# Performance work log

Measured on AMD Instinct MI355X. Metric: run time of the kernel, lower is better.

Reference implementation:

```python
import jax, jax.numpy as jnp
import numpy as np

TEMP = 0.07
WEIGHT = 0.5
EPS = 1e-8  # matches torch F.cosine_similarity norm clamp


def setup_inputs() -> dict:
    key = jax.random.key(0)
    k1, k2, k3 = jax.random.split(key, 3)
    B, T, D = 64, 512, 512
    video = jax.random.normal(k1, (B, T, D), dtype=jnp.float32)
    audio = jax.random.normal(k2, (B, T, D), dtype=jnp.float32)
    mask = jax.random.randint(k3, (B, T), 0, 2, dtype=jnp.int32)
    return {"video": video, "audio": audio, "mask": mask}


def reference(video, audio, mask):
    B, T, D = video.shape
    # L2-normalize features (cosine similarity = dot of normalized vectors)
    vn = video / jnp.clip(jnp.linalg.norm(video, axis=-1, keepdims=True), EPS)
    an = audio / jnp.clip(jnp.linalg.norm(audio, axis=-1, keepdims=True), EPS)
    idx = jnp.argmax(mask, axis=1)                                   # [B]
    a_anchor = jnp.take_along_axis(an, idx[:, None, None], axis=1)[:, 0]  # [B,D]
    v_anchor = jnp.take_along_axis(vn, idx[:, None, None], axis=1)[:, 0]  # [B,D]
    # scaled cosine sims of all timesteps vs the anchor of the other modality
    sims_a2v = jnp.einsum('btd,bd->bt', vn, a_anchor) / TEMP         # cos(v_j, a_idx)/T
    sims_v2a = jnp.einsum('btd,bd->bt', an, v_anchor) / TEMP         # cos(a_j, v_idx)/T
    # positive: cos(v_idx, a_idx)/T (same for both directions)
    pos = jnp.take_along_axis(sims_a2v, idx[:, None], axis=1)[:, 0]  # [B]
    not_pos = jnp.arange(T)[None, :] != idx[:, None]                 # [B,T]
    neg_a = jnp.sum(jnp.where(not_pos, jnp.exp(sims_a2v), 0.0), axis=1)  # a2v negatives
    neg_v = jnp.sum(jnp.where(not_pos, jnp.exp(sims_v2a), 0.0), axis=1)  # v2a negatives
    pos_exp = jnp.exp(pos)
    batch_loss_a = jnp.sum(-jnp.log(pos_exp / neg_a))
    batch_loss_v = jnp.sum(-jnp.log(pos_exp / neg_v))
    return ((batch_loss_a * WEIGHT + batch_loss_v * WEIGHT) / B).reshape(1)
```

## Files before the change

### kernel.cpp

```cpp
#include <hip/hip_runtime.h>
#include <math.h>

#define TEMP_INV (1.0f / 0.07f)
#define WEIGHT 0.5f
#define EPS 1e-8f
#define BB 64
#define TT 512
#define DD 512
#define RR 4
#define NC 4
#define ROWS_PER_WAVE (RR * NC)
#define XBLK (TT / (4 * ROWS_PER_WAVE))
#define NBLK (XBLK * BB * 2)
#define IDX_INF 0x7fffffff

typedef float f32x4 __attribute__((ext_vector_type(4)));

__device__ inline float wave_sum(float v) {
    for (int o = 32; o >= 1; o >>= 1) v += __shfl_xor(v, o, 64);
    return v;
}
__device__ inline int wave_min_i(int v) {
    for (int o = 32; o >= 1; o >>= 1) v = min(v, __shfl_xor(v, o, 64));
    return v;
}

#define LOADC(B0, B1, CH)                                                   \
    _Pragma("unroll")                                                       \
    for (int r = 0; r < RR; r++) {                                          \
        const float* row_ = base + (size_t)(t0 + (CH) * RR + r) * DD;       \
        B0[r] = *(const f32x4*)(row_ + lane * 4);                           \
        B1[r] = *(const f32x4*)(row_ + 256 + lane * 4);                     \
    }

#define COMPC(B0, B1, CH)                                                   \
    _Pragma("unroll")                                                       \
    for (int r = 0; r < RR; r++) {                                          \
        const int k_ = (CH) * RR + r;                                       \
        dot[k_] = B0[r].x * c0.x + B0[r].y * c0.y + B0[r].z * c0.z          \
                + B0[r].w * c0.w + B1[r].x * c1.x + B1[r].y * c1.y          \
                + B1[r].z * c1.z + B1[r].w * c1.w;                          \
        nrm[k_] = B0[r].x * B0[r].x + B0[r].y * B0[r].y + B0[r].z * B0[r].z \
                + B0[r].w * B0[r].w + B1[r].x * B1[r].x + B1[r].y * B1[r].y \
                + B1[r].z * B1[r].z + B1[r].w * B1[r].w;                    \
    }

__global__ __launch_bounds__(256) void fused_kernel(
    const float* __restrict__ video, const float* __restrict__ audio,
    const int* __restrict__ mask,
    float* __restrict__ pos, float* __restrict__ part,
    unsigned int* __restrict__ counter, float* __restrict__ out)
{
    const int b = blockIdx.y;
    const int dir = blockIdx.z;
    const int tid = threadIdx.x;
    const int wid = tid >> 6, lane = tid & 63;
    const int t0 = blockIdx.x * (4 * ROWS_PER_WAVE) + wid * ROWS_PER_WAVE;

    __shared__ int sh_i[4];
    __shared__ float sh_f[4][3];
    __shared__ int s_idx;
    __shared__ float s_anc[DD];
    __shared__ float s_inv;
    __shared__ int s_last;

    const float* base = (dir == 0 ? video : audio) + (size_t)b * TT * DD;

    int m0 = mask[b * TT + tid];
    int m1 = mask[b * TT + tid + 256];

    f32x4 pa0[RR], pa1[RR], pb0[RR], pb1[RR];
    LOADC(pa0, pa1, 0)
    LOADC(pb0, pb1, 1)
    asm volatile("" ::: "memory");

    int cand = min(m0 ? tid : IDX_INF, m1 ? (tid + 256) : IDX_INF);
    cand = wave_min_i(cand);
    if (lane == 0) sh_i[wid] = cand;
    __syncthreads();
    if (tid == 0) {
        int r = sh_i[0];
        for (int i = 1; i < 4; i++) r = min(r, sh_i[i]);
        s_idx = (r == IDX_INF) ? 0 : r;
    }
    __syncthreads();
    const int idx = s_idx;

    const float* ancrow = (dir == 0 ? audio : video) + (size_t)(b * TT + idx) * DD;

    float a0 = ancrow[tid], a1 = ancrow[tid + 256];
    s_anc[tid] = a0;
    s_anc[tid + 256] = a1;
    float ss = a0 * a0 + a1 * a1;
    float sso = 0.0f, dav = 0.0f;
    const bool posduty = (blockIdx.x == 0) && (dir == 0);
    ss = wave_sum(ss);
    if (posduty) {
        const float* vrow = video + (size_t)(b * TT + idx) * DD;
        float o0 = vrow[tid], o1 = vrow[tid + 256];
        sso = wave_sum(o0 * o0 + o1 * o1);
        dav = wave_sum(a0 * o0 + a1 * o1);
    }
    if (lane == 0) { sh_f[wid][0] = ss; sh_f[wid][1] = sso; sh_f[wid][2] = dav; }
    __syncthreads();
    if (tid == 0) {
        float ra = 0.f, ro = 0.f, rd = 0.f;
        for (int i = 0; i < 4; i++) { ra += sh_f[i][0]; ro += sh_f[i][1]; rd += sh_f[i][2]; }
        float inva = 1.0f / fmaxf(sqrtf(ra), EPS);
        s_inv = inva;
        if (posduty) {
            float invo = 1.0f / fmaxf(sqrtf(ro), EPS);
            __hip_atomic_store(&pos[b], rd * inva * invo * TEMP_INV,
                               __ATOMIC_RELAXED, __HIP_MEMORY_SCOPE_AGENT);
        }
    }
    __syncthreads();
    const float inv = s_inv;
    f32x4 c0 = ((const f32x4*)s_anc)[lane] * inv;
    f32x4 c1 = ((const f32x4*)(s_anc + 256))[lane] * inv;

    float dot[ROWS_PER_WAVE], nrm[ROWS_PER_WAVE];

    COMPC(pa0, pa1, 0)
    LOADC(pa0, pa1, 2)
    COMPC(pb0, pb1, 1)
    LOADC(pb0, pb1, 3)
    COMPC(pa0, pa1, 2)
    COMPC(pb0, pb1, 3)

#pragma unroll
    for (int o = 32; o >= 1; o >>= 1) {
#pragma unroll
        for (int k = 0; k < ROWS_PER_WAVE; k++) {
            dot[k] += __shfl_xor(dot[k], o, 64);
            nrm[k] += __shfl_xor(nrm[k], o, 64);
        }
    }

    if (lane == 0) {
        float local = 0.0f;
#pragma unroll
        for (int k = 0; k < ROWS_PER_WAVE; k++) {
            const int t = t0 + k;
            float sim = dot[k] / fmaxf(sqrtf(nrm[k]), EPS) * TEMP_INV;
            local += (t == idx) ? 0.0f : expf(sim);
        }
        sh_f[wid][0] = local;
    }
    __syncthreads();
    if (tid == 0) {
        float p = sh_f[0][0] + sh_f[1][0] + sh_f[2][0] + sh_f[3][0];
        const int bid_flat = (dir * BB + b) * XBLK + blockIdx.x;
        __hip_atomic_store(&part[bid_flat], p,
                           __ATOMIC_RELAXED, __HIP_MEMORY_SCOPE_AGENT);
        asm volatile("s_waitcnt vmcnt(0)" ::: "memory");
        unsigned old = __hip_atomic_fetch_add(counter, 1u,
                                              __ATOMIC_RELAXED, __HIP_MEMORY_SCOPE_AGENT);
        s_last = (old == (unsigned)(NBLK - 1)) ? 1 : 0;
    }
    __syncthreads();
    if (s_last && wid == 0) {
        float na = 0.f, nv = 0.f;
#pragma unroll
        for (int x = 0; x < XBLK; x++)
            na += __hip_atomic_load(&part[(0 * BB + lane) * XBLK + x],
                                    __ATOMIC_RELAXED, __HIP_MEMORY_SCOPE_AGENT);
#pragma unroll
        for (int x = 0; x < XBLK; x++)
            nv += __hip_atomic_load(&part[(1 * BB + lane) * XBLK + x],
                                    __ATOMIC_RELAXED, __HIP_MEMORY_SCOPE_AGENT);
        float p = __hip_atomic_load(&pos[lane],
                                    __ATOMIC_RELAXED, __HIP_MEMORY_SCOPE_AGENT);
        float term = WEIGHT * (logf(na) + logf(nv)) - p;
        term = wave_sum(term);
        if (lane == 0) out[0] = term * (1.0f / (float)BB);
    }
}

extern "C" void kernel_launch(void* const* d_in, const int* in_sizes, int n_in,
                              void* d_out, int out_size, void* d_ws, size_t ws_size,
                              hipStream_t stream)
{
    const float* video = (const float*)d_in[0];
    const float* audio = (const float*)d_in[1];
    const int* mask = (const int*)d_in[2];

    float* ws = (float*)d_ws;
    float* pos = ws;
    float* part = ws + BB;
    unsigned int* counter = (unsigned int*)(part + NBLK);

    hipMemsetAsync(counter, 0, sizeof(unsigned int), stream);

    dim3 grid(XBLK, BB, 2);
    fused_kernel<<<grid, 256, 0, stream>>>(video, audio, mask, pos, part, counter, (float*)d_out);
}
```

Baseline: 158.2 us.

## Split feature dimension across wave pairs and halve rows per block

Each block now covers 32 timesteps instead of 64, which doubles the grid. Wave pairs split the 512-wide feature dimension in half, and their partial dot products and norms are combined through shared memory before the exp. The aim is more resident waves and fewer registers per wave, so more memory parallelism can hide load latency. The row prefetch that used to be issued before the mask argmin and anchor normalisation now starts only after them, so that overlap is lost. Mask and anchor reads repeat in twice as many blocks.

```diff
diff --git a/kernel.cpp b/kernel.cpp
--- a/kernel.cpp
+++ b/kernel.cpp
@@ -8,9 +8,9 @@
 #define TT 512
 #define DD 512
 #define RR 4
-#define NC 4
-#define ROWS_PER_WAVE (RR * NC)
-#define XBLK (TT / (4 * ROWS_PER_WAVE))
+#define KROWS 16
+#define TROWS 32
+#define XBLK (TT / TROWS)
 #define NBLK (XBLK * BB * 2)
 #define IDX_INF 0x7fffffff
 
@@ -25,24 +25,20 @@
     return v;
 }
 
-#define LOADC(B0, B1, CH)                                                   \
+#define LOADC(BUF, CH)                                                      \
     _Pragma("unroll")                                                       \
     for (int r = 0; r < RR; r++) {                                          \
-        const float* row_ = base + (size_t)(t0 + (CH) * RR + r) * DD;       \
-        B0[r] = *(const f32x4*)(row_ + lane * 4);                           \
-        B1[r] = *(const f32x4*)(row_ + 256 + lane * 4);                     \
+        BUF[r] = *(const f32x4*)(base + (size_t)(rbase + (CH) * RR + r) * DD + coff); \
     }
 
-#define COMPC(B0, B1, CH)                                                   \
+#define COMPC(BUF, CH)                                                      \
     _Pragma("unroll")                                                       \
     for (int r = 0; r < RR; r++) {                                          \
         const int k_ = (CH) * RR + r;                                       \
-        dot[k_] = B0[r].x * c0.x + B0[r].y * c0.y + B0[r].z * c0.z          \
-                + B0[r].w * c0.w + B1[r].x * c1.x + B1[r].y * c1.y          \
-                + B1[r].z * c1.z + B1[r].w * c1.w;                          \
-        nrm[k_] = B0[r].x * B0[r].x + B0[r].y * B0[r].y + B0[r].z * B0[r].z \
-                + B0[r].w * B0[r].w + B1[r].x * B1[r].x + B1[r].y * B1[r].y \
-                + B1[r].z * B1[r].z + B1[r].w * B1[r].w;                    \
+        dot[k_] = BUF[r].x * c.x + BUF[r].y * c.y                           \
+                + BUF[r].z * c.z + BUF[r].w * c.w;                          \
+        nrm[k_] = BUF[r].x * BUF[r].x + BUF[r].y * BUF[r].y                 \
+                + BUF[r].z * BUF[r].z + BUF[r].w * BUF[r].w;                \
     }
 
 __global__ __launch_bounds__(256) void fused_kernel(
@@ -55,10 +51,13 @@
     const int dir = blockIdx.z;
     const int tid = threadIdx.x;
     const int wid = tid >> 6, lane = tid & 63;
-    const int t0 = blockIdx.x * (4 * ROWS_PER_WAVE) + wid * ROWS_PER_WAVE;
+    const int half = wid & 1;
+    const int rbase = blockIdx.x * TROWS + (wid >> 1) * KROWS;
+    const int coff = half * 256 + lane * 4;
 
     __shared__ int sh_i[4];
     __shared__ float sh_f[4][3];
+    __shared__ float s_red[4][KROWS][2];
     __shared__ int s_idx;
     __shared__ float s_anc[DD];
     __shared__ float s_inv;
@@ -68,33 +67,24 @@
 
     int m0 = mask[b * TT + tid];
     int m1 = mask[b * TT + tid + 256];
-
-    f32x4 pa0[RR], pa1[RR], pb0[RR], pb1[RR];
-    LOADC(pa0, pa1, 0)
-    LOADC(pb0, pb1, 1)
-    asm volatile("" ::: "memory");
-
     int cand = min(m0 ? tid : IDX_INF, m1 ? (tid + 256) : IDX_INF);
     cand = wave_min_i(cand);
     if (lane == 0) sh_i[wid] = cand;
     __syncthreads();
     if (tid == 0) {
-        int r = sh_i[0];
-        for (int i = 1; i < 4; i++) r = min(r, sh_i[i]);
+        int r = min(min(sh_i[0], sh_i[1]), min(sh_i[2], sh_i[3]));
         s_idx = (r == IDX_INF) ? 0 : r;
     }
     __syncthreads();
     const int idx = s_idx;
 
     const float* ancrow = (dir == 0 ? audio : video) + (size_t)(b * TT + idx) * DD;
-
     float a0 = ancrow[tid], a1 = ancrow[tid + 256];
     s_anc[tid] = a0;
     s_anc[tid + 256] = a1;
-    float ss = a0 * a0 + a1 * a1;
+    float ss = wave_sum(a0 * a0 + a1 * a1);
     float sso = 0.0f, dav = 0.0f;
     const bool posduty = (blockIdx.x == 0) && (dir == 0);
-    ss = wave_sum(ss);
     if (posduty) {
         const float* vrow = video + (size_t)(b * TT + idx) * DD;
         float o0 = vrow[tid], o1 = vrow[tid + 256];
@@ -116,40 +106,52 @@
     }
     __syncthreads();
     const float inv = s_inv;
-    f32x4 c0 = ((const f32x4*)s_anc)[lane] * inv;
-    f32x4 c1 = ((const f32x4*)(s_anc + 256))[lane] * inv;
+    f32x4 c = ((const f32x4*)s_anc)[half * 64 + lane] * inv;
 
-    float dot[ROWS_PER_WAVE], nrm[ROWS_PER_WAVE];
+    f32x4 pa[RR], pb[RR];
+    float dot[KROWS], nrm[KROWS];
 
-    COMPC(pa0, pa1, 0)
-    LOADC(pa0, pa1, 2)
-    COMPC(pb0, pb1, 1)
-    LOADC(pb0, pb1, 3)
-    COMPC(pa0, pa1, 2)
-    COMPC(pb0, pb1, 3)
+    LOADC(pa, 0)
+    LOADC(pb, 1)
+    COMPC(pa, 0)
+    LOADC(pa, 2)
+    COMPC(pb, 1)
+    LOADC(pb, 3)
+    COMPC(pa, 2)
+    COMPC(pb, 3)
 
 #pragma unroll
     for (int o = 32; o >= 1; o >>= 1) {
 #pragma unroll
-        for (int k = 0; k < ROWS_PER_WAVE; k++) {
+        for (int k = 0; k < KROWS; k++) {
             dot[k] += __shfl_xor(dot[k], o, 64);
             nrm[k] += __shfl_xor(nrm[k], o, 64);
         }
     }
 
     if (lane == 0) {
+#pragma unroll
+        for (int k = 0; k < KROWS; k++) {
+            s_red[wid][k][0] = dot[k];
+            s_red[wid][k][1] = nrm[k];
+        }
+    }
+    __syncthreads();
+    if (half == 0 && lane == 0) {
         float local = 0.0f;
 #pragma unroll
-        for (int k = 0; k < ROWS_PER_WAVE; k++) {
-            const int t = t0 + k;
-            float sim = dot[k] / fmaxf(sqrtf(nrm[k]), EPS) * TEMP_INV;
+        for (int k = 0; k < KROWS; k++) {
+            float d = s_red[wid][k][0] + s_red[wid + 1][k][0];
+            float n = s_red[wid][k][1] + s_red[wid + 1][k][1];
+            const int t = rbase + k;
+            float sim = d / fmaxf(sqrtf(n), EPS) * TEMP_INV;
             local += (t == idx) ? 0.0f : expf(sim);
         }
         sh_f[wid][0] = local;
     }
     __syncthreads();
     if (tid == 0) {
-        float p = sh_f[0][0] + sh_f[1][0] + sh_f[2][0] + sh_f[3][0];
+        float p = sh_f[0][0] + sh_f[2][0];
         const int bid_flat = (dir * BB + b) * XBLK + blockIdx.x;
         __hip_atomic_store(&part[bid_flat], p,
                            __ATOMIC_RELAXED, __HIP_MEMORY_SCOPE_AGENT);
```

Result: no change. 158.4 us (+0.1%).
